# Kernel optimization log

Measured on AMD Instinct MI355X. Metric: run time of the kernel, lower is better.

## Reference

```python
import jax, jax.numpy as jnp
import numpy as np

N_FREQ = 7  # freqs = 2**linspace(0, 6, 7) == 2**arange(7)
SKIP = (4,)


def nerf_encode(p):
    # nerfstudio NeRFEncoding with include_input=True, windows_param=None
    freqs = 2.0 ** jnp.arange(N_FREQ, dtype=p.dtype)          # [7]
    scaled = (2.0 * jnp.pi) * p                               # [N,3]
    s = (scaled[..., None] * freqs).reshape(p.shape[0], -1)   # [N,21]
    enc = jnp.sin(jnp.concatenate([s, s + 0.5 * jnp.pi], axis=-1))  # [N,42] = sin | cos
    return jnp.concatenate([enc, p], axis=-1)                 # [N,45]


def _hat_pt3d(w):
    # pytorch3d hat convention (transpose of the standard skew matrix)
    x, y, z = w[:, 0], w[:, 1], w[:, 2]
    o = jnp.zeros_like(x)
    return jnp.stack([
        jnp.stack([o, z, -y], -1),
        jnp.stack([-z, o, x], -1),
        jnp.stack([y, -x, o], -1)], -2)                       # [N,3,3]


def se3_exp_map_T(screw, eps=1e-4):
    # pytorch3d.transforms.se3_exp_map(screw).permute(0, 2, 1)
    v, w = screw[:, :3], screw[:, 3:]
    ang2 = jnp.clip(jnp.sum(w * w, axis=-1), eps, None)
    ang = jnp.sqrt(ang2)
    K = _hat_pt3d(w)
    KK = jnp.matmul(K, K)
    f1 = (jnp.sin(ang) / ang)[:, None, None]
    f2 = ((1.0 - jnp.cos(ang)) / ang2)[:, None, None]
    f3 = ((ang - jnp.sin(ang)) / (ang * ang2))[:, None, None]
    I = jnp.eye(3, dtype=screw.dtype)
    R = I + f1 * K + f2 * KK       # pytorch3d (row-vector) rotation
    V = I + f2 * K + f3 * KK
    T = jnp.einsum('nij,nj->ni', V, v)
    M = jnp.zeros((screw.shape[0], 4, 4), screw.dtype)
    M = M.at[:, :3, :3].set(jnp.swapaxes(R, -1, -2))  # transpose of [[R,0],[T,1]]
    M = M.at[:, :3, 3].set(T)
    M = M.at[:, 3, 3].set(1.0)
    return M


def mlp_stem(x, Ws, bs):
    inp = x
    n = len(Ws)
    for i in range(n):
        if i in SKIP:
            x = jnp.concatenate([inp, x], axis=-1)
        x = x @ Ws[i].T + bs[i]
        x = jax.nn.relu(x)  # hidden activation; i==n-1 is out_activation (also ReLU)
    return x


def setup_inputs() -> dict:
    key = jax.random.key(0)
    ks = jax.random.split(key, 16)
    N = 524288
    d = {
        'positions': jax.random.uniform(ks[0], (N, 3), jnp.float32),
        'directions': jax.random.normal(ks[1], (N, 3), jnp.float32),
        'warp_code': jax.random.normal(ks[2], (N, 8), jnp.float32),
    }
    fan_ins = [53, 128, 128, 128, 181, 128]
    for i, fi in enumerate(fan_ins):
        d[f'W{i}'] = jax.random.normal(ks[3 + i], (128, fi), jnp.float32) / np.sqrt(fi)
        d[f'b{i}'] = jnp.zeros((128,), jnp.float32)
    d['Wr'] = jax.random.normal(ks[10], (3, 128), jnp.float32) * 1e-5
    d['br'] = jnp.zeros((3,), jnp.float32)
    d['Wv'] = jax.random.normal(ks[11], (3, 128), jnp.float32) * 1e-5
    d['bv'] = jnp.zeros((3,), jnp.float32)
    return d


def reference(positions, directions, warp_code,
              W0, b0, W1, b1, W2, b2, W3, b3, W4, b4, W5, b5,
              Wr, br, Wv, bv):
    enc = nerf_encode(positions)                                  # [N,45]
    feat = mlp_stem(jnp.concatenate([enc, warp_code], axis=-1),
                    [W0, W1, W2, W3, W4, W5], [b0, b1, b2, b3, b4, b5])  # [N,128]
    r = feat @ Wr.T + br                                          # [N,3]
    v = feat @ Wv.T + bv                                          # [N,3]
    screw = jnp.concatenate([v, r], axis=-1)                      # [N,6]
    M = se3_exp_map_T(screw)                                      # [N,4,4]
    ph = jnp.concatenate([positions, jnp.ones_like(positions[:, :1])], axis=-1)
    wp_h = jnp.einsum('nij,nj->ni', M, ph)                        # [N,4]
    wp = wp_h[:, :3] / wp_h[:, 3:]
    wp = jnp.where(jnp.isnan(wp), positions, wp)
    rots = M[:, :3, :3]
    wd = jnp.einsum('nij,nj->ni', rots, directions)
    wd = jnp.where(jnp.isnan(wd), directions, wd)
    return wp, wd
```

## Files before the change

### kernel.cpp

```cpp
#include <hip/hip_runtime.h>
#include <hip/hip_bf16.h>
#include <hip/hip_fp8.h>
#include <math.h>


typedef float f32x4 __attribute__((ext_vector_type(4)));

#define NROWS 524288
#define BROWS 256

#define P0 0
#define P1 8192
#define P2 24576
#define P3 40960
#define P4 57344
#define P5 81920
#define PH 98304
#define PTOT 100352

#define QINV (1.0f / 4096.0f)

#define X0_OFF   0
#define XA_OFF   16384
#define BIAS_OFF 49152
#define SC_OFF   0
#define LDS_SZ   52352

template<int KS, int FAN>
__device__ __forceinline__ float pack_val(const float* __restrict__ W, int idx)
{
    int f  = idx / (KS * 512);
    int r2 = idx % (KS * 512);
    int s  = r2 >> 9, r3 = r2 & 511, ln = r3 >> 3, j = r3 & 7;
    int col = f * 16 + (ln & 15);
    int k   = s * 32 + (ln >> 4) * 8 + j;
    if (FAN == 128) return W[col * 128 + k];
    if (FAN == 53)  return (k < 53) ? W[col * 53 + k] : 0.f;
    if (k < 53)  return W[col * 181 + k];
    if (k < 64)  return 0.f;
    return W[col * 181 + (k - 11)];
}

__global__ void pack_w(const float* __restrict__ W0, const float* __restrict__ W1,
                       const float* __restrict__ W2, const float* __restrict__ W3,
                       const float* __restrict__ W4, const float* __restrict__ W5,
                       const float* __restrict__ Wr, const float* __restrict__ Wv,
                       unsigned char* __restrict__ pk)
{
    int e = blockIdx.x * 256 + threadIdx.x;
    if (e >= PTOT) return;
    float val;
    if (e >= PH) {
        int rem = e - PH;
        int s = rem >> 9, r3 = rem & 511, ln = r3 >> 3, j = r3 & 7;
        int col = ln & 15;
        int k = s * 32 + (ln >> 4) * 8 + j;
        if (col < 3)      val = Wv[col * 128 + k] * 4096.f;
        else if (col < 6) val = Wr[(col - 3) * 128 + k] * 4096.f;
        else              val = 0.f;
    }
    else if (e < P1) val = pack_val<2, 53 >(W0, e - P0);
    else if (e < P2) val = pack_val<4, 128>(W1, e - P1);
    else if (e < P3) val = pack_val<4, 128>(W2, e - P2);
    else if (e < P4) val = pack_val<4, 128>(W3, e - P3);
    else if (e < P5) val = pack_val<6, 181>(W4, e - P4);
    else             val = pack_val<4, 128>(W5, e - P5);
    pk[e] = (unsigned char)__hip_cvt_float_to_fp8(val, __HIP_SATFINITE, __HIP_E4M3);
}

__device__ __forceinline__ unsigned cvt4_fp8(float a, float b, float c, float d)
{
#if __has_builtin(__builtin_amdgcn_cvt_pk_fp8_f32)
    int v = __builtin_amdgcn_cvt_pk_fp8_f32(a, b, 0, false);
    v = __builtin_amdgcn_cvt_pk_fp8_f32(c, d, v, true);
    return (unsigned)v;
#else
    float2 ab; ab.x = a; ab.y = b;
    float2 cd; cd.x = c; cd.y = d;
    unsigned lo = (unsigned)__hip_cvt_float2_to_fp8x2(ab, __HIP_SATFINITE, __HIP_E4M3);
    unsigned hi = (unsigned)__hip_cvt_float2_to_fp8x2(cd, __HIP_SATFINITE, __HIP_E4M3);
    return lo | (hi << 16);
#endif
}

__device__ __forceinline__ float fsin01(float t) {
    float r; asm("v_sin_f32 %0, %1" : "=v"(r) : "v"(t)); return r;
}
__device__ __forceinline__ float fcos01(float t) {
    float r; asm("v_cos_f32 %0, %1" : "=v"(r) : "v"(t)); return r;
}

template<int KS, int SPLIT, bool BAR1>
__device__ __forceinline__ void mlp_layer(
    unsigned char* smem, const unsigned char* __restrict__ pkL, int lyr,
    const int* bA, const int* sB,
    int lane, int c, int g, int mfG, int nfG)
{
    f32x4 acc[4][4];
    #pragma unroll
    for (int mf = 0; mf < 4; mf++) {
        f32x4 bb = *(const f32x4*)(smem + BIAS_OFF
                       + (lyr * 128 + mfG * 64 + mf * 16 + g * 4) * 4);
        #pragma unroll
        for (int nf = 0; nf < 4; nf++) acc[mf][nf] = bb;
    }

    const unsigned long long* pA = (const unsigned long long*)pkL;
    #pragma unroll
    for (int s = 0; s < KS; s++) {
        unsigned long long Af[4];
        #pragma unroll
        for (int mf = 0; mf < 4; mf++)
            Af[mf] = pA[((mfG * 4 + mf) * KS + s) * 64 + lane];
        unsigned long long Bf[4];
        #pragma unroll
        for (int nf = 0; nf < 4; nf++) {
            if (s < SPLIT) {
                int row = 64 * nfG + 16 * nf + c;
                Bf[nf] = *(const unsigned long long*)(smem + X0_OFF + row * 64
                              + ((32 * s + 8 * g) ^ ((row & 7) << 3)));
            } else {
                Bf[nf] = *(const unsigned long long*)(smem
                              + (bA[nf] ^ (32 * (s - SPLIT))));
            }
        }
        #pragma unroll
        for (int mf = 0; mf < 4; mf++)
            #pragma unroll
            for (int nf = 0; nf < 4; nf++)
                acc[mf][nf] = __builtin_amdgcn_mfma_f32_16x16x32_fp8_fp8(
                    (long)Af[mf], (long)Bf[nf], acc[mf][nf], 0, 0, 0);
    }

    if (BAR1) __syncthreads();

    #pragma unroll
    for (int mf = 0; mf < 4; mf++)
        #pragma unroll
        for (int nf = 0; nf < 4; nf++) {
            f32x4 a = acc[mf][nf];
            unsigned d = cvt4_fp8(fmaxf(a[0], 0.f), fmaxf(a[1], 0.f),
                                  fmaxf(a[2], 0.f), fmaxf(a[3], 0.f));
            *(unsigned*)(smem + (sB[nf] ^ (16 * mf))) = d;
        }
    __syncthreads();
}

__global__ __launch_bounds__(512, 4)
void se3_fused(const float* __restrict__ pos, const float* __restrict__ dir,
               const float* __restrict__ wcode,
               const float* __restrict__ b0, const float* __restrict__ b1,
               const float* __restrict__ b2, const float* __restrict__ b3,
               const float* __restrict__ b4, const float* __restrict__ b5,
               const float* __restrict__ br, const float* __restrict__ bv,
               const unsigned char* __restrict__ pk,
               float* __restrict__ out)
{
    __shared__ unsigned char smem[LDS_SZ];
    const int tid  = threadIdx.x;
    const int lane = tid & 63;
    const int w    = tid >> 6;
    const int c    = lane & 15;
    const int g    = lane >> 4;
    const int mfG  = w & 1;
    const int nfG  = w >> 1;
    const int r0   = blockIdx.x * BROWS;

    int bA[4], sB[4];
    #pragma unroll
    for (int nf = 0; nf < 4; nf++) {
        int row = 64 * nfG + 16 * nf + c;
        int sw  = (row & 15) << 3;
        bA[nf] = XA_OFF + row * 128 + ((8 * g) ^ (sw & 0x18)) + (sw & 0x60);
        sB[nf] = XA_OFF + row * 128 + ((64 * mfG + 4 * g) ^ sw);
    }

    for (int i = tid; i < 800; i += 512) {
        float v;
        if (i < 768) {
            int l = i >> 7, m = i & 127;
            const float* bp = (l == 0) ? b0 : (l == 1) ? b1 : (l == 2) ? b2
                           : (l == 3) ? b3 : (l == 4) ? b4 : b5;
            v = bp[m];
        } else {
            int m = i - 768;
            v = (m < 3) ? bv[m] : ((m < 6) ? br[m - 3] : 0.f);
        }
        *(float*)(smem + BIAS_OFF + i * 4) = v;
    }

    {
        int row = tid >> 1, h = tid & 1;
        int gg = r0 + row;
        float p0 = pos[gg*3+0], p1 = pos[gg*3+1], p2 = pos[gg*3+2];
        float vals[32];
        if (h == 0) {
            #pragma unroll
            for (int j = 0; j < 21; j++) {
                float p = (j < 7) ? p0 : (j < 14 ? p1 : p2);
                float t = p * (float)(1 << (j % 7));
                t -= floorf(t);
                vals[j] = fsin01(t);
            }
            #pragma unroll
            for (int j = 21; j < 32; j++) {
                int idx = j - 21;
                float p = (idx < 7) ? p0 : (idx < 14 ? p1 : p2);
                float t = p * (float)(1 << (idx % 7));
                t -= floorf(t);
                vals[j] = fcos01(t);
            }
        } else {
            #pragma unroll
            for (int j = 0; j < 10; j++) {
                int idx = 11 + j;
                float p = (idx < 14) ? p1 : p2;
                float t = p * (float)(1 << (idx % 7));
                t -= floorf(t);
                vals[j] = fcos01(t);
            }
            vals[10] = p0; vals[11] = p1; vals[12] = p2;
            const float4* wc4 = (const float4*)(wcode + (size_t)gg * 8);
            float4 wa = wc4[0], wb = wc4[1];
            vals[13] = wa.x; vals[14] = wa.y; vals[15] = wa.z; vals[16] = wa.w;
            vals[17] = wb.x; vals[18] = wb.y; vals[19] = wb.z; vals[20] = wb.w;
            #pragma unroll
            for (int j = 21; j < 32; j++) vals[j] = 0.f;
        }
        unsigned dw[8];
        #pragma unroll
        for (int q = 0; q < 8; q++)
            dw[q] = cvt4_fp8(vals[4*q], vals[4*q+1], vals[4*q+2], vals[4*q+3]);
        int swx = (row & 7) << 3;
        unsigned char* base = smem + X0_OFF + row * 64;
        #pragma unroll
        for (int i = 0; i < 4; i++) {
            uint2 u; u.x = dw[2*i]; u.y = dw[2*i+1];
            *(uint2*)(base + ((32 * h + 8 * i) ^ swx)) = u;
        }
    }
    __syncthreads();

    mlp_layer<2,2,false>(smem, pk + P0, 0, bA, sB, lane, c, g, mfG, nfG);
    mlp_layer<4,0,true >(smem, pk + P1, 1, bA, sB, lane, c, g, mfG, nfG);
    mlp_layer<4,0,true >(smem, pk + P2, 2, bA, sB, lane, c, g, mfG, nfG);
    mlp_layer<4,0,true >(smem, pk + P3, 3, bA, sB, lane, c, g, mfG, nfG);
    mlp_layer<6,2,true >(smem, pk + P4, 4, bA, sB, lane, c, g, mfG, nfG);
    mlp_layer<4,0,true >(smem, pk + P5, 5, bA, sB, lane, c, g, mfG, nfG);

    if (mfG == 0) {
        const unsigned long long* pA = (const unsigned long long*)(pk + PH);
        f32x4 ha[4];
        #pragma unroll
        for (int nf = 0; nf < 4; nf++) ha[nf] = f32x4{0.f, 0.f, 0.f, 0.f};
        #pragma unroll
        for (int s = 0; s < 4; s++) {
            unsigned long long Ah = pA[s * 64 + lane];
            #pragma unroll
            for (int nf = 0; nf < 4; nf++) {
                unsigned long long Bf = *(const unsigned long long*)(smem
                                           + (bA[nf] ^ (32 * s)));
                ha[nf] = __builtin_amdgcn_mfma_f32_16x16x32_fp8_fp8(
                    (long)Ah, (long)Bf, ha[nf], 0, 0, 0);
            }
        }
        f32x4 hb = *(const f32x4*)(smem + BIAS_OFF + (768 + g * 4) * 4);
        #pragma unroll
        for (int nf = 0; nf < 4; nf++) {
            int row = 64 * nfG + 16 * nf + c;
            if (g == 0) {
                f32x4 sc;
                #pragma unroll
                for (int r = 0; r < 4; r++) sc[r] = ha[nf][r] * QINV + hb[r];
                *(f32x4*)(smem + SC_OFF + row * 32) = sc;
            } else if (g == 1) {
                float* sp = (float*)(smem + SC_OFF + row * 32);
                sp[4] = ha[nf][0] * QINV + hb[0];
                sp[5] = ha[nf][1] * QINV + hb[1];
            }
        }
    }
    __syncthreads();

    if (tid < BROWS) {
        int row = tid, gg = r0 + row;
        const float* sc = (const float*)(smem + SC_OFF + row * 32);
        float v0 = sc[0], v1 = sc[1], v2 = sc[2];
        float wx = sc[3], wy = sc[4], wz = sc[5];
        float ang2 = wx*wx + wy*wy + wz*wz;
        ang2 = fmaxf(ang2, 1e-4f);
        float ang = sqrtf(ang2);
        float sn = __sinf(ang), cs = __cosf(ang);
        float f1 = sn / ang;
        float f2 = (1.f - cs) / ang2;
        float f3 = (ang - sn) / (ang * ang2);
        float K[3][3] = {{0.f,  wz, -wy}, {-wz, 0.f,  wx}, { wy, -wx, 0.f}};
        float KK[3][3];
        #pragma unroll
        for (int i = 0; i < 3; i++)
            #pragma unroll
            for (int j = 0; j < 3; j++)
                KK[i][j] = K[i][0]*K[0][j] + K[i][1]*K[1][j] + K[i][2]*K[2][j];
        float R[3][3], V[3][3];
        #pragma unroll
        for (int i = 0; i < 3; i++)
            #pragma unroll
            for (int j = 0; j < 3; j++) {
                float id = (i == j) ? 1.f : 0.f;
                R[i][j] = id + f1 * K[i][j] + f2 * KK[i][j];
                V[i][j] = id + f2 * K[i][j] + f3 * KK[i][j];
            }
        float T0 = V[0][0]*v0 + V[0][1]*v1 + V[0][2]*v2;
        float T1 = V[1][0]*v0 + V[1][1]*v1 + V[1][2]*v2;
        float T2 = V[2][0]*v0 + V[2][1]*v1 + V[2][2]*v2;
        float px = pos[gg*3+0], py = pos[gg*3+1], pz = pos[gg*3+2];
        float dx = dir[gg*3+0], dy = dir[gg*3+1], dz = dir[gg*3+2];
        float wpx = R[0][0]*px + R[1][0]*py + R[2][0]*pz + T0;
        float wpy = R[0][1]*px + R[1][1]*py + R[2][1]*pz + T1;
        float wpz = R[0][2]*px + R[1][2]*py + R[2][2]*pz + T2;
        float wdx = R[0][0]*dx + R[1][0]*dy + R[2][0]*dz;
        float wdy = R[0][1]*dx + R[1][1]*dy + R[2][1]*dz;
        float wdz = R[0][2]*dx + R[1][2]*dy + R[2][2]*dz;
        wpx = (wpx != wpx) ? px : wpx;
        wpy = (wpy != wpy) ? py : wpy;
        wpz = (wpz != wpz) ? pz : wpz;
        wdx = (wdx != wdx) ? dx : wdx;
        wdy = (wdy != wdy) ? dy : wdy;
        wdz = (wdz != wdz) ? dz : wdz;
        out[gg*3+0] = wpx; out[gg*3+1] = wpy; out[gg*3+2] = wpz;
        float* o2 = out + (size_t)NROWS * 3;
        o2[gg*3+0] = wdx; o2[gg*3+1] = wdy; o2[gg*3+2] = wdz;
    }
}

extern "C" void kernel_launch(void* const* d_in, const int* in_sizes, int n_in,
                              void* d_out, int out_size, void* d_ws, size_t ws_size,
                              hipStream_t stream)
{
    const float* pos = (const float*)d_in[0];
    const float* dir = (const float*)d_in[1];
    const float* wc  = (const float*)d_in[2];
    const float* W0 = (const float*)d_in[3];  const float* b0 = (const float*)d_in[4];
    const float* W1 = (const float*)d_in[5];  const float* b1 = (const float*)d_in[6];
    const float* W2 = (const float*)d_in[7];  const float* b2 = (const float*)d_in[8];
    const float* W3 = (const float*)d_in[9];  const float* b3 = (const float*)d_in[10];
    const float* W4 = (const float*)d_in[11]; const float* b4 = (const float*)d_in[12];
    const float* W5 = (const float*)d_in[13]; const float* b5 = (const float*)d_in[14];
    const float* Wr = (const float*)d_in[15]; const float* br = (const float*)d_in[16];
    const float* Wv = (const float*)d_in[17]; const float* bv = (const float*)d_in[18];
    unsigned char* pkb = (unsigned char*)d_ws;
    float* out = (float*)d_out;

    pack_w<<<(PTOT + 255) / 256, 256, 0, stream>>>(W0, W1, W2, W3, W4, W5, Wr, Wv, pkb);
    se3_fused<<<NROWS / BROWS, 512, 0, stream>>>(pos, dir, wc,
                                                 b0, b1, b2, b3, b4, b5,
                                                 br, bv, pkb, out);
}
```

Before: 246.3 us.

## Shrink fused MLP blocks to 64 rows with 4 waves and smaller LDS

Block size drops from 256 rows/512 threads to 64 rows/256 threads. Each wave now owns 32 output features for all 64 rows, so it holds 8 accumulators instead of 16. Biases are read directly from global memory instead of being staged in LDS, and the encoding work is spread over 4 threads per row. Each block now needs far less LDS and fewer registers, which should allow more resident blocks and shorter per-block barriers. The trade-off is that each weight fragment is reused across fewer rows, so weights are fetched from cache more often, and the grid has four times as many blocks.

New measurement: 203.1 us. 1.21x faster.

```diff
diff --git a/kernel.cpp b/kernel.cpp
--- a/kernel.cpp
+++ b/kernel.cpp
@@ -5,9 +5,10 @@
 
 
 typedef float f32x4 __attribute__((ext_vector_type(4)));
+typedef unsigned long long u64;
 
 #define NROWS 524288
-#define BROWS 256
+#define BROWS 64
 
 #define P0 0
 #define P1 8192
@@ -20,11 +21,10 @@
 
 #define QINV (1.0f / 4096.0f)
 
-#define X0_OFF   0
-#define XA_OFF   16384
-#define BIAS_OFF 49152
-#define SC_OFF   0
-#define LDS_SZ   52352
+#define X0_OFF 0
+#define XA_OFF 4096
+#define SC_OFF 0
+#define LDS_SZ 12288
 
 template<int KS, int FAN>
 __device__ __forceinline__ float pack_val(const float* __restrict__ W, int idx)
@@ -89,43 +89,45 @@
 __device__ __forceinline__ float fcos01(float t) {
     float r; asm("v_cos_f32 %0, %1" : "=v"(r) : "v"(t)); return r;
 }
+__device__ __forceinline__ float enc_sin(float p, int f) {
+    float t = p * (float)(1 << f); t -= floorf(t); return fsin01(t);
+}
+__device__ __forceinline__ float enc_cos(float p, int f) {
+    float t = p * (float)(1 << f); t -= floorf(t); return fcos01(t);
+}
 
 template<int KS, int SPLIT, bool BAR1>
 __device__ __forceinline__ void mlp_layer(
-    unsigned char* smem, const unsigned char* __restrict__ pkL, int lyr,
-    const int* bA, const int* sB,
-    int lane, int c, int g, int mfG, int nfG)
-{
-    f32x4 acc[4][4];
+    unsigned char* smem, const unsigned char* __restrict__ pkL,
+    const float* __restrict__ bl,
+    const int* bA, const int* sB, const int* x0A,
+    int lane, int g, int w)
+{
+    f32x4 acc[2][4];
     #pragma unroll
-    for (int mf = 0; mf < 4; mf++) {
-        f32x4 bb = *(const f32x4*)(smem + BIAS_OFF
-                       + (lyr * 128 + mfG * 64 + mf * 16 + g * 4) * 4);
+    for (int mf = 0; mf < 2; mf++) {
+        f32x4 bb = *(const f32x4*)(bl + 32 * w + 16 * mf + 4 * g);
         #pragma unroll
         for (int nf = 0; nf < 4; nf++) acc[mf][nf] = bb;
     }
 
-    const unsigned long long* pA = (const unsigned long long*)pkL;
+    const u64* pA = (const u64*)pkL;
     #pragma unroll
     for (int s = 0; s < KS; s++) {
-        unsigned long long Af[4];
-        #pragma unroll
-        for (int mf = 0; mf < 4; mf++)
-            Af[mf] = pA[((mfG * 4 + mf) * KS + s) * 64 + lane];
-        unsigned long long Bf[4];
+        u64 Af[2];
+        #pragma unroll
+        for (int mf = 0; mf < 2; mf++)
+            Af[mf] = pA[((w * 2 + mf) * KS + s) * 64 + lane];
+        u64 Bf[4];
         #pragma unroll
         for (int nf = 0; nf < 4; nf++) {
-            if (s < SPLIT) {
-                int row = 64 * nfG + 16 * nf + c;
-                Bf[nf] = *(const unsigned long long*)(smem + X0_OFF + row * 64
-                              + ((32 * s + 8 * g) ^ ((row & 7) << 3)));
-            } else {
-                Bf[nf] = *(const unsigned long long*)(smem
-                              + (bA[nf] ^ (32 * (s - SPLIT))));
-            }
-        }
-        #pragma unroll
-        for (int mf = 0; mf < 4; mf++)
+            if (s < SPLIT)
+                Bf[nf] = *(const u64*)(smem + (x0A[nf] ^ (32 * s)));
+            else
+                Bf[nf] = *(const u64*)(smem + (bA[nf] ^ (32 * (s - SPLIT))));
+        }
+        #pragma unroll
+        for (int mf = 0; mf < 2; mf++)
             #pragma unroll
             for (int nf = 0; nf < 4; nf++)
                 acc[mf][nf] = __builtin_amdgcn_mfma_f32_16x16x32_fp8_fp8(
@@ -135,7 +137,7 @@
     if (BAR1) __syncthreads();
 
     #pragma unroll
-    for (int mf = 0; mf < 4; mf++)
+    for (int mf = 0; mf < 2; mf++)
         #pragma unroll
         for (int nf = 0; nf < 4; nf++) {
             f32x4 a = acc[mf][nf];
@@ -146,7 +148,7 @@
     __syncthreads();
 }
 
-__global__ __launch_bounds__(512, 4)
+__global__ __launch_bounds__(256, 4)
 void se3_fused(const float* __restrict__ pos, const float* __restrict__ dir,
                const float* __restrict__ wcode,
                const float* __restrict__ b0, const float* __restrict__ b1,
@@ -162,121 +164,106 @@
     const int w    = tid >> 6;
     const int c    = lane & 15;
     const int g    = lane >> 4;
-    const int mfG  = w & 1;
-    const int nfG  = w >> 1;
     const int r0   = blockIdx.x * BROWS;
 
-    int bA[4], sB[4];
+    int bA[4], sB[4], x0A[4];
     #pragma unroll
     for (int nf = 0; nf < 4; nf++) {
-        int row = 64 * nfG + 16 * nf + c;
-        int sw  = (row & 15) << 3;
-        bA[nf] = XA_OFF + row * 128 + ((8 * g) ^ (sw & 0x18)) + (sw & 0x60);
-        sB[nf] = XA_OFF + row * 128 + ((64 * mfG + 4 * g) ^ sw);
-    }
-
-    for (int i = tid; i < 800; i += 512) {
-        float v;
-        if (i < 768) {
-            int l = i >> 7, m = i & 127;
-            const float* bp = (l == 0) ? b0 : (l == 1) ? b1 : (l == 2) ? b2
-                           : (l == 3) ? b3 : (l == 4) ? b4 : b5;
-            v = bp[m];
-        } else {
-            int m = i - 768;
-            v = (m < 3) ? bv[m] : ((m < 6) ? br[m - 3] : 0.f);
-        }
-        *(float*)(smem + BIAS_OFF + i * 4) = v;
+        int row = 16 * nf + c;
+        int sw4 = (row & 15) << 3;
+        int sw3 = (row & 7) << 3;
+        bA[nf]  = XA_OFF + row * 128 + ((8 * g) ^ sw4);
+        sB[nf]  = XA_OFF + row * 128 + ((32 * w + 4 * g) ^ sw4);
+        x0A[nf] = X0_OFF + row * 64  + ((8 * g) ^ sw3);
     }
 
     {
-        int row = tid >> 1, h = tid & 1;
+        int row = tid >> 2, h = tid & 3;
         int gg = r0 + row;
         float p0 = pos[gg*3+0], p1 = pos[gg*3+1], p2 = pos[gg*3+2];
-        float vals[32];
+        float vals[16];
         if (h == 0) {
             #pragma unroll
-            for (int j = 0; j < 21; j++) {
-                float p = (j < 7) ? p0 : (j < 14 ? p1 : p2);
-                float t = p * (float)(1 << (j % 7));
-                t -= floorf(t);
-                vals[j] = fsin01(t);
-            }
-            #pragma unroll
-            for (int j = 21; j < 32; j++) {
-                int idx = j - 21;
-                float p = (idx < 7) ? p0 : (idx < 14 ? p1 : p2);
-                float t = p * (float)(1 << (idx % 7));
-                t -= floorf(t);
-                vals[j] = fcos01(t);
-            }
-        } else {
-            #pragma unroll
-            for (int j = 0; j < 10; j++) {
-                int idx = 11 + j;
-                float p = (idx < 14) ? p1 : p2;
-                float t = p * (float)(1 << (idx % 7));
-                t -= floorf(t);
-                vals[j] = fcos01(t);
-            }
+            for (int f = 0; f < 7; f++) vals[f]     = enc_sin(p0, f);
+            #pragma unroll
+            for (int f = 0; f < 7; f++) vals[7+f]   = enc_sin(p1, f);
+            #pragma unroll
+            for (int f = 0; f < 2; f++) vals[14+f]  = enc_sin(p2, f);
+        } else if (h == 1) {
+            #pragma unroll
+            for (int f = 2; f < 7; f++) vals[f-2]   = enc_sin(p2, f);
+            #pragma unroll
+            for (int f = 0; f < 7; f++) vals[5+f]   = enc_cos(p0, f);
+            #pragma unroll
+            for (int f = 0; f < 4; f++) vals[12+f]  = enc_cos(p1, f);
+        } else if (h == 2) {
+            #pragma unroll
+            for (int f = 4; f < 7; f++) vals[f-4]   = enc_cos(p1, f);
+            #pragma unroll
+            for (int f = 0; f < 7; f++) vals[3+f]   = enc_cos(p2, f);
             vals[10] = p0; vals[11] = p1; vals[12] = p2;
             const float4* wc4 = (const float4*)(wcode + (size_t)gg * 8);
+            float4 wa = wc4[0];
+            vals[13] = wa.x; vals[14] = wa.y; vals[15] = wa.z;
+        } else {
+            const float4* wc4 = (const float4*)(wcode + (size_t)gg * 8);
             float4 wa = wc4[0], wb = wc4[1];
-            vals[13] = wa.x; vals[14] = wa.y; vals[15] = wa.z; vals[16] = wa.w;
-            vals[17] = wb.x; vals[18] = wb.y; vals[19] = wb.z; vals[20] = wb.w;
-            #pragma unroll
-            for (int j = 21; j < 32; j++) vals[j] = 0.f;
-        }
-        unsigned dw[8];
-        #pragma unroll
-        for (int q = 0; q < 8; q++)
+            vals[0] = wa.w;
+            vals[1] = wb.x; vals[2] = wb.y; vals[3] = wb.z; vals[4] = wb.w;
+            #pragma unroll
+            for (int q = 5; q < 16; q++) vals[q] = 0.f;
+        }
+        unsigned dw[4];
+        #pragma unroll
+        for (int q = 0; q < 4; q++)
             dw[q] = cvt4_fp8(vals[4*q], vals[4*q+1], vals[4*q+2], vals[4*q+3]);
-        int swx = (row & 7) << 3;
+        int sw = (row & 7) << 3;
         unsigned char* base = smem + X0_OFF + row * 64;
-        #pragma unroll
-        for (int i = 0; i < 4; i++) {
-            uint2 u; u.x = dw[2*i]; u.y = dw[2*i+1];
-            *(uint2*)(base + ((32 * h + 8 * i) ^ swx)) = u;
-        }
+        uint2 ua; ua.x = dw[0]; ua.y = dw[1];
+        uint2 ub; ub.x = dw[2]; ub.y = dw[3];
+        *(uint2*)(base + ((16 * h)     ^ sw)) = ua;
+        *(uint2*)(base + ((16 * h + 8) ^ sw)) = ub;
     }
     __syncthreads();
 
-    mlp_layer<2,2,false>(smem, pk + P0, 0, bA, sB, lane, c, g, mfG, nfG);
-    mlp_layer<4,0,true >(smem, pk + P1, 1, bA, sB, lane, c, g, mfG, nfG);
-    mlp_layer<4,0,true >(smem, pk + P2, 2, bA, sB, lane, c, g, mfG, nfG);
-    mlp_layer<4,0,true >(smem, pk + P3, 3, bA, sB, lane, c, g, mfG, nfG);
-    mlp_layer<6,2,true >(smem, pk + P4, 4, bA, sB, lane, c, g, mfG, nfG);
-    mlp_layer<4,0,true >(smem, pk + P5, 5, bA, sB, lane, c, g, mfG, nfG);
-
-    if (mfG == 0) {
-        const unsigned long long* pA = (const unsigned long long*)(pk + PH);
+    mlp_layer<2,2,false>(smem, pk + P0, b0, bA, sB, x0A, lane, g, w);
+    mlp_layer<4,0,true >(smem, pk + P1, b1, bA, sB, x0A, lane, g, w);
+    mlp_layer<4,0,true >(smem, pk + P2, b2, bA, sB, x0A, lane, g, w);
+    mlp_layer<4,0,true >(smem, pk + P3, b3, bA, sB, x0A, lane, g, w);
+    mlp_layer<6,2,true >(smem, pk + P4, b4, bA, sB, x0A, lane, g, w);
+    mlp_layer<4,0,true >(smem, pk + P5, b5, bA, sB, x0A, lane, g, w);
+
+    if (w == 0) {
+        const u64* pA = (const u64*)(pk + PH);
         f32x4 ha[4];
         #pragma unroll
         for (int nf = 0; nf < 4; nf++) ha[nf] = f32x4{0.f, 0.f, 0.f, 0.f};
         #pragma unroll
         for (int s = 0; s < 4; s++) {
-            unsigned long long Ah = pA[s * 64 + lane];
+            u64 Ah = pA[s * 64 + lane];
             #pragma unroll
             for (int nf = 0; nf < 4; nf++) {
-                unsigned long long Bf = *(const unsigned long long*)(smem
-                                           + (bA[nf] ^ (32 * s)));
+                u64 Bf = *(const u64*)(smem + (bA[nf] ^ (32 * s)));
                 ha[nf] = __builtin_amdgcn_mfma_f32_16x16x32_fp8_fp8(
                     (long)Ah, (long)Bf, ha[nf], 0, 0, 0);
             }
         }
-        f32x4 hb = *(const f32x4*)(smem + BIAS_OFF + (768 + g * 4) * 4);
+        float bv0 = bv[0], bv1 = bv[1], bv2 = bv[2];
+        float br0 = br[0], br1 = br[1], br2 = br[2];
         #pragma unroll
         for (int nf = 0; nf < 4; nf++) {
-            int row = 64 * nfG + 16 * nf + c;
+            int row = 16 * nf + c;
             if (g == 0) {
-                f32x4 sc;
-                #pragma unroll
-                for (int r = 0; r < 4; r++) sc[r] = ha[nf][r] * QINV + hb[r];
-                *(f32x4*)(smem + SC_OFF + row * 32) = sc;
+                f32x4 scv;
+                scv[0] = ha[nf][0] * QINV + bv0;
+                scv[1] = ha[nf][1] * QINV + bv1;
+                scv[2] = ha[nf][2] * QINV + bv2;
+                scv[3] = ha[nf][3] * QINV + br0;
+                *(f32x4*)(smem + SC_OFF + row * 32) = scv;
             } else if (g == 1) {
                 float* sp = (float*)(smem + SC_OFF + row * 32);
-                sp[4] = ha[nf][0] * QINV + hb[0];
-                sp[5] = ha[nf][1] * QINV + hb[1];
+                sp[4] = ha[nf][0] * QINV + br1;
+                sp[5] = ha[nf][1] * QINV + br2;
             }
         }
     }
@@ -352,7 +339,7 @@
     float* out = (float*)d_out;
 
     pack_w<<<(PTOT + 255) / 256, 256, 0, stream>>>(W0, W1, W2, W3, W4, W5, Wr, Wv, pkb);
-    se3_fused<<<NROWS / BROWS, 512, 0, stream>>>(pos, dir, wc,
+    se3_fused<<<NROWS / BROWS, 256, 0, stream>>>(pos, dir, wc,
                                                  b0, b1, b2, b3, b4, b5,
                                                  br, bv, pkb, out);
 }
```
